# Kernel optimization log

Hardware: AMD Instinct MI355X
Metric: run time of the kernel (lower is better)

Reference implementation:

```python
import jax, jax.numpy as jnp
import numpy as np

B, N, C_IN, H, S, K = 32, 1024, 2, 32, 2, 2  # batch, nodes, input feat, hidden, n_supports, k_hop
NUM_MAT = S * K + 1  # identity + K hops per support


def setup_inputs() -> dict:
    key = jax.random.key(0)
    ks = jax.random.split(key, 6)
    inputs = jax.random.normal(ks[0], (B, N, C_IN), dtype=jnp.float32)
    # dense diffusion supports, scaled ~1/N so k-hop products stay O(1) (row-stochastic-like)
    supports = jax.random.uniform(ks[1], (B, S, N, N), dtype=jnp.float32) * (2.0 / N)
    states = jax.random.normal(ks[2], (B, N, H), dtype=jnp.float32)
    c_cat = C_IN + H
    scale = 1.0 / np.sqrt(NUM_MAT * c_cat)
    W_ru = jax.random.normal(ks[3], (NUM_MAT * c_cat, 2 * H), dtype=jnp.float32) * scale
    b_ru = jnp.zeros((2 * H,), dtype=jnp.float32)
    W_c = jax.random.normal(ks[4], (NUM_MAT * c_cat, H), dtype=jnp.float32) * scale
    b_c = jnp.zeros((H,), dtype=jnp.float32)
    return {"inputs": inputs, "supports": supports, "states": states,
            "W_ru": W_ru, "b_ru": b_ru, "W_c": W_c, "b_c": b_c}


def _graph_conv(x, supports, W, b):
    # x: [B,N,C]; supports: [B,S,N,N]. DCRNN dense diffusion conv:
    feats = [x]
    for s in range(S):
        A = supports[:, s]  # [B,N,N]
        xk = x
        for _ in range(K):
            xk = jnp.einsum('bnm,bmc->bnc', A, xk)
            feats.append(xk)
    h = jnp.concatenate(feats, axis=-1)  # [B,N,NUM_MAT*C]
    return jnp.einsum('bnf,fo->bno', h, W) + b


def reference(inputs, supports, states, W_ru, b_ru, W_c, b_c):
    r_u = jax.nn.sigmoid(_graph_conv(jnp.concatenate([inputs, states], -1), supports, W_ru, b_ru))
    r, u = r_u[..., :H], r_u[..., H:]
    c = jnp.tanh(_graph_conv(jnp.concatenate([inputs, r * states], -1), supports, W_c, b_c))
    outputs = u * states + (1.0 - u) * c
    return (outputs, outputs)
```

## Files before the change

### kernel.cpp

```cpp
#include <hip/hip_runtime.h>


#define NN   1024
#define HB   245760
#define SUBT 16384
#define OUTCOPY 1048576

typedef float  f32x4  __attribute__((ext_vector_type(4)));
typedef short  s16x4  __attribute__((ext_vector_type(4)));
typedef short  s16x8  __attribute__((ext_vector_type(8)));
typedef __bf16 bf16x8 __attribute__((ext_vector_type(8)));
typedef unsigned int u32x4 __attribute__((ext_vector_type(4)));

#define GAS __attribute__((address_space(1)))
#define LAS __attribute__((address_space(3)))

__device__ __forceinline__ unsigned short f32_bf16(float f) {
  unsigned int u = __float_as_uint(f);
  u += 0x7FFFu + ((u >> 16) & 1u);
  return (unsigned short)(u >> 16);
}
__device__ __forceinline__ float bf16_f32(unsigned short h) {
  return __uint_as_float(((unsigned int)h) << 16);
}

__device__ __forceinline__ void gload_lds16(const unsigned short* g, void* l) {
  __builtin_amdgcn_global_load_lds((const GAS void*)g, (LAS void*)l, 16, 0, 0);
}

__global__ __launch_bounds__(256)
void cvt_bf16(const float* __restrict__ src, unsigned short* __restrict__ dst, int n4) {
  int i = blockIdx.x * 256 + threadIdx.x;
  int stride = gridDim.x * 256;
  for (; i < n4; i += stride) {
    float4 v = ((const float4*)src)[i];
    s16x4 o;
    o.x = (short)f32_bf16(v.x);
    o.y = (short)f32_bf16(v.y);
    o.z = (short)f32_bf16(v.z);
    o.w = (short)f32_bf16(v.w);
    ((s16x4*)dst)[i] = o;
  }
}

__global__ __launch_bounds__(256)
void pack_x1(const float* __restrict__ inputs, const float* __restrict__ states,
             unsigned short* __restrict__ H1) {
  int gid = blockIdx.x * 256 + threadIdx.x;
  int b = gid >> 10, n = gid & 1023;
  unsigned short* xb = H1 + (size_t)b * HB;
  xb[0 * NN + n] = f32_bf16(inputs[gid * 2 + 0]);
  xb[1 * NN + n] = f32_bf16(inputs[gid * 2 + 1]);
#pragma unroll
  for (int o = 0; o < 32; ++o) {
    int ch = 2 + o;
    xb[(ch >> 4) * SUBT + (ch & 15) * NN + n] = f32_bf16(states[gid * 32 + o]);
  }
#pragma unroll
  for (int ch = 34; ch < 48; ++ch)
    xb[2 * SUBT + (ch & 15) * NN + n] = 0;
}

__global__ __launch_bounds__(256, 4)
void hop_fast(const unsigned short* __restrict__ Abf,
              const unsigned short* __restrict__ Hin,
              unsigned short* __restrict__ Hout,
              int si0, int si1, int so0, int so1) {
  __shared__ u32x4 lds4[2][896];

  const int tid  = threadIdx.x;
  const int wave = tid >> 6, lane = tid & 63;
  const int l15  = lane & 15,  l4  = lane >> 4;
  const int mblk = blockIdx.x, b = blockIdx.y, s = blockIdx.z;
  const int slot_in  = s ? si1 : si0;
  const int slot_out = s ? so1 : so0;

  const unsigned short* Xb = Hin  + (size_t)b * HB + (size_t)slot_in  * 3 * SUBT;
  unsigned short*       Yb = Hout + (size_t)b * HB + (size_t)slot_out * 3 * SUBT;
  const size_t arow0 = ((size_t)(b * 2 + s) * NN + (size_t)mblk * 64) * NN;

  f32x4 acc[3];
#pragma unroll
  for (int nt = 0; nt < 3; ++nt)
#pragma unroll
    for (int e = 0; e < 4; ++e) acc[nt][e] = 0.f;

  auto STAGE = [&](int bufi, int kb0) {
    char* base = (char*)&lds4[bufi][0];
#pragma unroll
    for (int i = 0; i < 2; ++i) {
      int q = i * 256 + tid;
      int r = q >> 3, cs = q & 7;
      const unsigned short* g = Abf + arow0 + (size_t)r * NN + kb0 + ((cs ^ (r & 7)) << 3);
      gload_lds16(g, base + (i * 256 + wave * 64) * 16);
    }
    {
      int q = tid;
      int ct = q >> 7, rem = q & 127, ch = rem >> 3, cs = rem & 7;
      const unsigned short* g = Xb + ct * SUBT + ch * NN + kb0 + ((cs ^ (ch & 7)) << 3);
      gload_lds16(g, base + 8192 + (wave * 64) * 16);
      if (wave < 2) {
        q = 256 + tid;
        ct = q >> 7; rem = q & 127; ch = rem >> 3; cs = rem & 7;
        g = Xb + ct * SUBT + ch * NN + kb0 + ((cs ^ (ch & 7)) << 3);
        gload_lds16(g, base + 8192 + (256 + wave * 64) * 16);
      }
    }
  };

  STAGE(0, 0);
  __syncthreads();

  const int row = wave * 16 + l15;
  const int sw  = (row & 7) << 4;
  const int swx = (l15 & 7) << 4;

  int cur = 0;
  for (int kt = 0; kt < 16; ++kt) {
    if (kt < 15) STAGE(cur ^ 1, (kt + 1) << 6);

    const char* lAb = (const char*)&lds4[cur][0];
    const char* lXb = lAb + 8192;

    __builtin_amdgcn_s_setprio(1);
#pragma unroll
    for (int kb = 0; kb < 2; ++kb) {
      const int ko = kb * 64 + (l4 << 3);
      s16x8 ta;
      ta.lo = *(const s16x4*)(lAb + row * 128 + (ko ^ sw));
      ta.hi = *(const s16x4*)(lAb + row * 128 + ((ko + 32) ^ sw));
      bf16x8 afr = __builtin_bit_cast(bf16x8, ta);
#pragma unroll
      for (int nt = 0; nt < 3; ++nt) {
        const char* bp = lXb + nt * 2048 + l15 * 128;
        s16x8 tb;
        tb.lo = *(const s16x4*)(bp + (ko ^ swx));
        tb.hi = *(const s16x4*)(bp + ((ko + 32) ^ swx));
        bf16x8 bfr = __builtin_bit_cast(bf16x8, tb);
        acc[nt] = __builtin_amdgcn_mfma_f32_16x16x32_bf16(afr, bfr, acc[nt], 0, 0, 0);
      }
    }
    __builtin_amdgcn_s_setprio(0);

    if (kt < 15) __syncthreads();
    cur ^= 1;
  }

  const int row0 = mblk * 64 + wave * 16 + (l4 << 2);
#pragma unroll
  for (int nt = 0; nt < 3; ++nt) {
    int ch = nt * 16 + l15;
    s16x4 o;
    o.x = (short)f32_bf16(acc[nt][0]);
    o.y = (short)f32_bf16(acc[nt][1]);
    o.z = (short)f32_bf16(acc[nt][2]);
    o.w = (short)f32_bf16(acc[nt][3]);
    *(s16x4*)(Yb + (size_t)ch * NN + row0) = o;
  }
}

__global__ __launch_bounds__(256)
void hop_slow(const float* __restrict__ Af32,
              const unsigned short* __restrict__ Hin,
              unsigned short* __restrict__ Hout,
              int si0, int si1, int so0, int so1) {
  __shared__ u32x4 lA4[1024];
  __shared__ u32x4 lX4[384];

  const int tid  = threadIdx.x;
  const int wave = tid >> 6, lane = tid & 63;
  const int l15  = lane & 15,  l4  = lane >> 4;
  const int mblk = blockIdx.x, b = blockIdx.y, s = blockIdx.z;
  const int slot_in  = s ? si1 : si0;
  const int slot_out = s ? so1 : so0;

  const unsigned short* Xb = Hin  + (size_t)b * HB + (size_t)slot_in  * 3 * SUBT;
  unsigned short*       Yb = Hout + (size_t)b * HB + (size_t)slot_out * 3 * SUBT;
  const size_t arow0 = ((size_t)(b * 2 + s) * NN + (size_t)mblk * 128) * NN;

  f32x4 acc[2][3];
#pragma unroll
  for (int mt = 0; mt < 2; ++mt)
#pragma unroll
    for (int nt = 0; nt < 3; ++nt)
#pragma unroll
      for (int e = 0; e < 4; ++e) acc[mt][nt][e] = 0.f;

  char* lAb = (char*)lA4;
  char* lXb = (char*)lX4;

  for (int kt = 0; kt < 16; ++kt) {
    const int kb0 = kt * 64;
    __syncthreads();
#pragma unroll
    for (int i = 0; i < 8; ++i) {
      int q = i * 256 + tid;
      int r = q >> 4, c = q & 15;
      float4 v = *(const float4*)(Af32 + arow0 + (size_t)r * NN + kb0 + c * 4);
      s16x4 o;
      o.x = (short)f32_bf16(v.x);
      o.y = (short)f32_bf16(v.y);
      o.z = (short)f32_bf16(v.z);
      o.w = (short)f32_bf16(v.w);
      *(s16x4*)(lAb + r * 128 + ((c * 8) ^ ((r & 7) << 4))) = o;
    }
    {
      int q = tid;
      int ct = q >> 7, rem = q & 127, ch = rem >> 3, c = rem & 7;
      const u32x4* src = (const u32x4*)(Xb + ct * SUBT + ch * NN + kb0 + c * 8);
      *(u32x4*)(lXb + ct * 2048 + ch * 128 + ((c ^ (ch & 7)) << 4)) = *src;
      if (tid < 128) {
        q = 256 + tid;
        ct = q >> 7; rem = q & 127; ch = rem >> 3; c = rem & 7;
        src = (const u32x4*)(Xb + ct * SUBT + ch * NN + kb0 + c * 8);
        *(u32x4*)(lXb + ct * 2048 + ch * 128 + ((c ^ (ch & 7)) << 4)) = *src;
      }
    }
    __syncthreads();
#pragma unroll
    for (int kb = 0; kb < 2; ++kb) {
      const int ko = kb * 64 + (l4 << 3);
      bf16x8 afr[2];
#pragma unroll
      for (int mt = 0; mt < 2; ++mt) {
        int row = wave * 32 + mt * 16 + l15;
        int sw  = (row & 7) << 4;
        s16x8 t;
        t.lo = *(const s16x4*)(lAb + row * 128 + (ko ^ sw));
        t.hi = *(const s16x4*)(lAb + row * 128 + ((ko + 32) ^ sw));
        afr[mt] = __builtin_bit_cast(bf16x8, t);
      }
#pragma unroll
      for (int nt = 0; nt < 3; ++nt) {
        const int swx = (l15 & 7) << 4;
        const char* bp = lXb + nt * 2048 + l15 * 128;
        s16x8 t;
        t.lo = *(const s16x4*)(bp + (ko ^ swx));
        t.hi = *(const s16x4*)(bp + ((ko + 32) ^ swx));
        bf16x8 bfr = __builtin_bit_cast(bf16x8, t);
#pragma unroll
        for (int mt = 0; mt < 2; ++mt)
          acc[mt][nt] = __builtin_amdgcn_mfma_f32_16x16x32_bf16(afr[mt], bfr, acc[mt][nt], 0, 0, 0);
      }
    }
  }

#pragma unroll
  for (int mt = 0; mt < 2; ++mt)
#pragma unroll
    for (int nt = 0; nt < 3; ++nt) {
      int ch   = nt * 16 + l15;
      int row0 = mblk * 128 + wave * 32 + mt * 16 + (l4 << 2);
      s16x4 o;
      o.x = (short)f32_bf16(acc[mt][nt][0]);
      o.y = (short)f32_bf16(acc[mt][nt][1]);
      o.z = (short)f32_bf16(acc[mt][nt][2]);
      o.w = (short)f32_bf16(acc[mt][nt][3]);
      *(s16x4*)(Yb + (size_t)ch * NN + row0) = o;
    }
}

__global__ __launch_bounds__(256)
void gate_ru(const unsigned short* __restrict__ H1,
             const float* __restrict__ W, const float* __restrict__ bias,
             const float* __restrict__ inputs, const float* __restrict__ states,
             unsigned short* __restrict__ H2, float* __restrict__ ubuf) {
  int gid = blockIdx.x * 256 + threadIdx.x;
  int b = gid >> 10, n = gid & 1023;
  const unsigned short* hb = H1 + (size_t)b * HB;
  float acc[64];
#pragma unroll
  for (int o = 0; o < 64; ++o) acc[o] = bias[o];
  for (int j = 0; j < 5; ++j) {
    const unsigned short* sb = hb + j * 3 * SUBT;
    for (int c = 0; c < 34; ++c) {
      float xv = bf16_f32(sb[(c >> 4) * SUBT + (c & 15) * NN + n]);
      const float* wr = W + (j * 34 + c) * 64;
#pragma unroll
      for (int o = 0; o < 64; ++o) acc[o] = fmaf(xv, wr[o], acc[o]);
    }
  }
  unsigned short* xb = H2 + (size_t)b * HB;
  xb[0 * NN + n] = f32_bf16(inputs[gid * 2 + 0]);
  xb[1 * NN + n] = f32_bf16(inputs[gid * 2 + 1]);
#pragma unroll
  for (int o = 0; o < 32; ++o) {
    float r = 1.f / (1.f + __expf(-acc[o]));
    float u = 1.f / (1.f + __expf(-acc[32 + o]));
    float sv = states[gid * 32 + o];
    int ch = 2 + o;
    xb[(ch >> 4) * SUBT + (ch & 15) * NN + n] = f32_bf16(r * sv);
    ubuf[((size_t)b * 32 + o) * NN + n] = u;
  }
#pragma unroll
  for (int ch = 34; ch < 48; ++ch)
    xb[2 * SUBT + (ch & 15) * NN + n] = 0;
}

__global__ __launch_bounds__(256)
void gate_c(const unsigned short* __restrict__ H2,
            const float* __restrict__ W, const float* __restrict__ bias,
            const float* __restrict__ states, const float* __restrict__ ubuf,
            float* __restrict__ out) {
  int gid = blockIdx.x * 256 + threadIdx.x;
  int b = gid >> 10, n = gid & 1023;
  const unsigned short* hb = H2 + (size_t)b * HB;
  float acc[32];
#pragma unroll
  for (int o = 0; o < 32; ++o) acc[o] = bias[o];
  for (int j = 0; j < 5; ++j) {
    const unsigned short* sb = hb + j * 3 * SUBT;
    for (int c = 0; c < 34; ++c) {
      float xv = bf16_f32(sb[(c >> 4) * SUBT + (c & 15) * NN + n]);
      const float* wr = W + (j * 34 + c) * 32;
#pragma unroll
      for (int o = 0; o < 32; ++o) acc[o] = fmaf(xv, wr[o], acc[o]);
    }
  }
  float res[32];
#pragma unroll
  for (int o = 0; o < 32; ++o) {
    float cc = tanhf(acc[o]);
    float u  = ubuf[((size_t)b * 32 + o) * NN + n];
    float sv = states[gid * 32 + o];
    res[o] = u * sv + (1.f - u) * cc;
  }
  float* o0 = out + (size_t)gid * 32;
#pragma unroll
  for (int q = 0; q < 8; ++q) {
    f32x4 v = { res[q * 4 + 0], res[q * 4 + 1], res[q * 4 + 2], res[q * 4 + 3] };
    *(f32x4*)(o0 + q * 4) = v;
    *(f32x4*)(o0 + OUTCOPY + q * 4) = v;
  }
}

extern "C" void kernel_launch(void* const* d_in, const int* in_sizes, int n_in,
                              void* d_out, int out_size, void* d_ws, size_t ws_size,
                              hipStream_t stream) {
  (void)in_sizes; (void)n_in; (void)out_size;
  const float* inputs   = (const float*)d_in[0];
  const float* supports = (const float*)d_in[1];
  const float* states   = (const float*)d_in[2];
  const float* W_ru     = (const float*)d_in[3];
  const float* b_ru     = (const float*)d_in[4];
  const float* W_c      = (const float*)d_in[5];
  const float* b_c      = (const float*)d_in[6];
  float* out = (float*)d_out;

  char* ws = (char*)d_ws;
  const size_t szA = 134217728;
  const size_t szH = 15728640;
  const size_t szU = 4194304;
  const bool pathA = ws_size >= szA + 2 * szH + szU;
  const size_t off = pathA ? szA : 0;

  unsigned short* Abf = (unsigned short*)ws;
  unsigned short* H1  = (unsigned short*)(ws + off);
  unsigned short* H2  = (unsigned short*)(ws + off + szH);
  float*          ub  = (float*)(ws + off + 2 * szH);

  dim3 fgrid(16, 32, 2), sgrid(8, 32, 2), blk(256);

  if (pathA)
    cvt_bf16<<<dim3(2048), blk, 0, stream>>>(supports, Abf, 16777216);

  pack_x1<<<dim3(128), blk, 0, stream>>>(inputs, states, H1);

  if (pathA) {
    hop_fast<<<fgrid, blk, 0, stream>>>(Abf, H1, H1, 0, 0, 1, 3);
    hop_fast<<<fgrid, blk, 0, stream>>>(Abf, H1, H1, 1, 3, 2, 4);
  } else {
    hop_slow<<<sgrid, blk, 0, stream>>>(supports, H1, H1, 0, 0, 1, 3);
    hop_slow<<<sgrid, blk, 0, stream>>>(supports, H1, H1, 1, 3, 2, 4);
  }

  gate_ru<<<dim3(128), blk, 0, stream>>>(H1, W_ru, b_ru, inputs, states, H2, ub);

  if (pathA) {
    hop_fast<<<fgrid, blk, 0, stream>>>(Abf, H2, H2, 0, 0, 1, 3);
    hop_fast<<<fgrid, blk, 0, stream>>>(Abf, H2, H2, 1, 3, 2, 4);
  } else {
    hop_slow<<<sgrid, blk, 0, stream>>>(supports, H2, H2, 0, 0, 1, 3);
    hop_slow<<<sgrid, blk, 0, stream>>>(supports, H2, H2, 1, 3, 2, 4);
  }

  gate_c<<<dim3(128), blk, 0, stream>>>(H2, W_c, b_c, states, ub, out);
}
```

Measured before the change: 320.6 us.

## Fuse all DCGRU stages into one persistent kernel with grid barriers

Replaces the sequence of separate launches (convert, pack, four hop GEMMs, two gate kernels) with a single persistent kernel of 256 blocks of 512 threads. The stages are separated by atomic-counter grid barriers. The hop phase now uses a 4-deep global-to-LDS pipeline with explicit waitcnt barriers, and each block computes two 128-row tiles. The gate stages are re-partitioned so that 8 threads share a node. The aim is to remove launch gaps and tail effects between the small kernels. The risks are deadlock if not all blocks are co-resident, spin-barrier overhead, and reduced occupancy.

```diff
diff --git a/kernel.cpp b/kernel.cpp
--- a/kernel.cpp
+++ b/kernel.cpp
@@ -23,23 +23,290 @@
 __device__ __forceinline__ float bf16_f32(unsigned short h) {
   return __uint_as_float(((unsigned int)h) << 16);
 }
-
 __device__ __forceinline__ void gload_lds16(const unsigned short* g, void* l) {
   __builtin_amdgcn_global_load_lds((const GAS void*)g, (LAS void*)l, 16, 0, 0);
 }
 
-__global__ __launch_bounds__(256)
-void cvt_bf16(const float* __restrict__ src, unsigned short* __restrict__ dst, int n4) {
-  int i = blockIdx.x * 256 + threadIdx.x;
-  int stride = gridDim.x * 256;
-  for (; i < n4; i += stride) {
-    float4 v = ((const float4*)src)[i];
-    s16x4 o;
-    o.x = (short)f32_bf16(v.x);
-    o.y = (short)f32_bf16(v.y);
-    o.z = (short)f32_bf16(v.z);
-    o.w = (short)f32_bf16(v.w);
-    ((s16x4*)dst)[i] = o;
+#define WB(N) do {                                              \
+    asm volatile("s_waitcnt vmcnt(" #N ") lgkmcnt(0)" ::: "memory"); \
+    __builtin_amdgcn_s_barrier();                               \
+    __builtin_amdgcn_sched_barrier(0);                          \
+  } while (0)
+
+__device__ __forceinline__ void gbar(unsigned* bar, unsigned target) {
+  __syncthreads();
+  if (threadIdx.x == 0) {
+    __threadfence();
+    __hip_atomic_fetch_add(bar, 1u, __ATOMIC_RELAXED, __HIP_MEMORY_SCOPE_AGENT);
+    unsigned v;
+    do {
+      __builtin_amdgcn_s_sleep(8);
+      v = __hip_atomic_load(bar, __ATOMIC_RELAXED, __HIP_MEMORY_SCOPE_AGENT);
+    } while (v < target);
+    __threadfence();
+  }
+  __syncthreads();
+}
+
+__device__ void hop_phase(const unsigned short* __restrict__ Abf,
+                          const unsigned short* __restrict__ Hin,
+                          unsigned short* __restrict__ Hout,
+                          int bs, int m0, char* lds,
+                          int si0, int si1, int so0, int so1) {
+  const int tid  = threadIdx.x;
+  const int wave = tid >> 6, lane = tid & 63;
+  const int l15  = lane & 15, l4 = lane >> 4;
+  const int b = bs & 31, s = bs >> 5;
+  const int slot_in  = s ? si1 : si0;
+  const int slot_out = s ? so1 : so0;
+
+  const unsigned short* Xb = Hin  + (size_t)b * HB + (size_t)slot_in  * 3 * SUBT;
+  unsigned short*       Yb = Hout + (size_t)b * HB + (size_t)slot_out * 3 * SUBT;
+  const size_t a0 = ((size_t)(b * 2 + s) * NN + (size_t)m0 * 128) * NN;
+  const size_t a1 = a0 + (size_t)4 * 128 * NN;
+
+  auto ISSUE = [&](int t) {
+    const int kt = t & 15, kb0 = kt << 6;
+    const size_t ar = (t >> 4) ? a1 : a0;
+    char* base = lds + (t & 3) * 24576;
+#pragma unroll
+    for (int i = 0; i < 2; ++i) {
+      int q = i * 512 + tid;
+      int r = q >> 3, cs = q & 7;
+      gload_lds16(Abf + ar + (size_t)r * NN + kb0 + ((cs ^ (r & 7)) << 3),
+                  base + (i * 512 + wave * 64) * 16);
+    }
+    {
+      int q = tid;
+      int ct = q >> 7, ch = (q >> 3) & 15, cs = q & 7;
+      gload_lds16(Xb + ct * SUBT + ch * NN + kb0 + ((cs ^ (ch & 7)) << 3),
+                  base + 16384 + (wave * 64) * 16);
+    }
+  };
+
+  const int row = wave * 16 + l15;
+  const int sw  = (row & 7) << 4;
+  const int swx = (l15 & 7) << 4;
+
+  f32x4 acc[3];
+#pragma unroll
+  for (int nt = 0; nt < 3; ++nt)
+#pragma unroll
+    for (int e = 0; e < 4; ++e) acc[nt][e] = 0.f;
+  s16x4 sv0[3];
+
+  auto COMPUTE = [&](int t) {
+    const char* lAb = lds + (t & 3) * 24576;
+    const char* lXb = lAb + 16384;
+#pragma unroll
+    for (int kb = 0; kb < 2; ++kb) {
+      const int ko = kb * 64 + (l4 << 3);
+      s16x8 ta;
+      ta.lo = *(const s16x4*)(lAb + row * 128 + (ko ^ sw));
+      ta.hi = *(const s16x4*)(lAb + row * 128 + ((ko + 32) ^ sw));
+      bf16x8 afr = __builtin_bit_cast(bf16x8, ta);
+#pragma unroll
+      for (int nt = 0; nt < 3; ++nt) {
+        const char* bp = lXb + nt * 2048 + l15 * 128;
+        s16x8 tb;
+        tb.lo = *(const s16x4*)(bp + (ko ^ swx));
+        tb.hi = *(const s16x4*)(bp + ((ko + 32) ^ swx));
+        bf16x8 bfr = __builtin_bit_cast(bf16x8, tb);
+        acc[nt] = __builtin_amdgcn_mfma_f32_16x16x32_bf16(afr, bfr, acc[nt], 0, 0, 0);
+      }
+    }
+  };
+
+  auto PACK = [&](s16x4* dst) {
+#pragma unroll
+    for (int nt = 0; nt < 3; ++nt) {
+      dst[nt].x = (short)f32_bf16(acc[nt][0]);
+      dst[nt].y = (short)f32_bf16(acc[nt][1]);
+      dst[nt].z = (short)f32_bf16(acc[nt][2]);
+      dst[nt].w = (short)f32_bf16(acc[nt][3]);
+    }
+  };
+
+  ISSUE(0); ISSUE(1); ISSUE(2);
+
+#pragma unroll 1
+  for (int k = 0; k < 30; ++k) {
+    WB(6);
+    if (k < 29) ISSUE(k + 3);
+    COMPUTE(k);
+    if (k == 15) {
+      PACK(sv0);
+#pragma unroll
+      for (int nt = 0; nt < 3; ++nt)
+#pragma unroll
+        for (int e = 0; e < 4; ++e) acc[nt][e] = 0.f;
+    }
+  }
+  WB(3); COMPUTE(30);
+  WB(0); COMPUTE(31);
+
+  s16x4 sv1[3];
+  PACK(sv1);
+
+  const int r0 = m0 * 128 + wave * 16 + (l4 << 2);
+  const int r1 = (m0 + 4) * 128 + wave * 16 + (l4 << 2);
+#pragma unroll
+  for (int nt = 0; nt < 3; ++nt) {
+    int ch = nt * 16 + l15;
+    *(s16x4*)(Yb + (size_t)ch * NN + r0) = sv0[nt];
+    *(s16x4*)(Yb + (size_t)ch * NN + r1) = sv1[nt];
+  }
+}
+
+__global__ __launch_bounds__(512, 2)
+void dcgru_fused(const float* __restrict__ inputs, const float* __restrict__ supports,
+                 const float* __restrict__ states,
+                 const float* __restrict__ W_ru, const float* __restrict__ b_ru,
+                 const float* __restrict__ W_c,  const float* __restrict__ b_c,
+                 float* __restrict__ out,
+                 unsigned short* __restrict__ Abf,
+                 unsigned short* __restrict__ H1, unsigned short* __restrict__ H2,
+                 float* __restrict__ ubuf, unsigned* bar) {
+  __shared__ u32x4 ldsv[6144];
+  char* lds = (char*)ldsv;
+
+  const int tid = threadIdx.x;
+  const int gid = blockIdx.x * 512 + tid;
+
+  const int x  = blockIdx.x & 7;
+  const int j  = blockIdx.x >> 3;
+  const int bs = x * 8 + (j >> 2);
+  const int m0 = j & 3;
+
+  {
+    const f32x4* src = (const f32x4*)supports;
+#pragma unroll 1
+    for (int i = gid; i < 16777216; i += 524288) {
+      f32x4 v0 = __builtin_nontemporal_load(src + i);
+      f32x4 v1 = __builtin_nontemporal_load(src + i + 131072);
+      f32x4 v2 = __builtin_nontemporal_load(src + i + 262144);
+      f32x4 v3 = __builtin_nontemporal_load(src + i + 393216);
+      s16x4 o0 = { (short)f32_bf16(v0[0]), (short)f32_bf16(v0[1]), (short)f32_bf16(v0[2]), (short)f32_bf16(v0[3]) };
+      s16x4 o1 = { (short)f32_bf16(v1[0]), (short)f32_bf16(v1[1]), (short)f32_bf16(v1[2]), (short)f32_bf16(v1[3]) };
+      s16x4 o2 = { (short)f32_bf16(v2[0]), (short)f32_bf16(v2[1]), (short)f32_bf16(v2[2]), (short)f32_bf16(v2[3]) };
+      s16x4 o3 = { (short)f32_bf16(v3[0]), (short)f32_bf16(v3[1]), (short)f32_bf16(v3[2]), (short)f32_bf16(v3[3]) };
+      ((s16x4*)Abf)[i] = o0;
+      ((s16x4*)Abf)[i + 131072] = o1;
+      ((s16x4*)Abf)[i + 262144] = o2;
+      ((s16x4*)Abf)[i + 393216] = o3;
+    }
+    if (gid < 32768) {
+      int b = gid >> 10, n = gid & 1023;
+      unsigned short* xb = H1 + (size_t)b * HB;
+      xb[0 * NN + n] = f32_bf16(inputs[gid * 2 + 0]);
+      xb[1 * NN + n] = f32_bf16(inputs[gid * 2 + 1]);
+#pragma unroll
+      for (int o = 0; o < 32; ++o) {
+        int ch = 2 + o;
+        xb[(ch >> 4) * SUBT + (ch & 15) * NN + n] = f32_bf16(states[gid * 32 + o]);
+      }
+#pragma unroll
+      for (int ch = 34; ch < 48; ++ch)
+        xb[2 * SUBT + (ch & 15) * NN + n] = 0;
+    }
+  }
+  gbar(bar, 256);
+
+  hop_phase(Abf, H1, H1, bs, m0, lds, 0, 0, 1, 3);
+  gbar(bar, 512);
+  hop_phase(Abf, H1, H1, bs, m0, lds, 1, 3, 2, 4);
+  gbar(bar, 768);
+
+  {
+#pragma unroll 1
+    for (int rep = 0; rep < 2; ++rep) {
+      int tau = gid + rep * 131072;
+      int rw = tau >> 3, p = tau & 7;
+      int b = rw >> 10, n = rw & 1023;
+      const unsigned short* hb = H1 + (size_t)b * HB;
+      float acc[8];
+#pragma unroll
+      for (int q = 0; q < 8; ++q) acc[q] = b_ru[p * 8 + q];
+#pragma unroll 1
+      for (int jj = 0; jj < 5; ++jj) {
+        const unsigned short* sb = hb + jj * 3 * SUBT;
+#pragma unroll 1
+        for (int c = 0; c < 34; ++c) {
+          float xv = bf16_f32(sb[(c >> 4) * SUBT + (c & 15) * NN + n]);
+          const float* wr = W_ru + (jj * 34 + c) * 64 + p * 8;
+          f32x4 w0 = *(const f32x4*)wr;
+          f32x4 w1 = *(const f32x4*)(wr + 4);
+#pragma unroll
+          for (int q = 0; q < 4; ++q) acc[q]     = fmaf(xv, w0[q], acc[q]);
+#pragma unroll
+          for (int q = 0; q < 4; ++q) acc[4 + q] = fmaf(xv, w1[q], acc[4 + q]);
+        }
+      }
+      unsigned short* xb = H2 + (size_t)b * HB;
+      if (p < 4) {
+#pragma unroll
+        for (int q = 0; q < 8; ++q) {
+          float r = 1.f / (1.f + __expf(-acc[q]));
+          int o = p * 8 + q, ch = 2 + o;
+          xb[(ch >> 4) * SUBT + (ch & 15) * NN + n] = f32_bf16(r * states[rw * 32 + o]);
+        }
+      } else {
+        int mm = (p - 4) * 8;
+#pragma unroll
+        for (int q = 0; q < 8; ++q) {
+          float u = 1.f / (1.f + __expf(-acc[q]));
+          ubuf[((size_t)b * 32 + mm + q) * NN + n] = u;
+        }
+      }
+      if (p == 4) { for (int ch = 34; ch < 41; ++ch) xb[2 * SUBT + (ch & 15) * NN + n] = 0; }
+      if (p == 5) { for (int ch = 41; ch < 48; ++ch) xb[2 * SUBT + (ch & 15) * NN + n] = 0; }
+      if (p == 6) {
+        xb[0 * NN + n] = f32_bf16(inputs[rw * 2 + 0]);
+        xb[1 * NN + n] = f32_bf16(inputs[rw * 2 + 1]);
+      }
+    }
+  }
+  gbar(bar, 1024);
+
+  hop_phase(Abf, H2, H2, bs, m0, lds, 0, 0, 1, 3);
+  gbar(bar, 1280);
+  hop_phase(Abf, H2, H2, bs, m0, lds, 1, 3, 2, 4);
+  gbar(bar, 1536);
+
+  {
+#pragma unroll 1
+    for (int rep = 0; rep < 2; ++rep) {
+      int tau = gid + rep * 131072;
+      int rw = tau >> 3, p = tau & 7;
+      int b = rw >> 10, n = rw & 1023;
+      const unsigned short* hb = H2 + (size_t)b * HB;
+      float acc[4];
+#pragma unroll
+      for (int q = 0; q < 4; ++q) acc[q] = b_c[p * 4 + q];
+#pragma unroll 1
+      for (int jj = 0; jj < 5; ++jj) {
+        const unsigned short* sb = hb + jj * 3 * SUBT;
+#pragma unroll 1
+        for (int c = 0; c < 34; ++c) {
+          float xv = bf16_f32(sb[(c >> 4) * SUBT + (c & 15) * NN + n]);
+          f32x4 w0 = *(const f32x4*)(W_c + (jj * 34 + c) * 32 + p * 4);
+#pragma unroll
+          for (int q = 0; q < 4; ++q) acc[q] = fmaf(xv, w0[q], acc[q]);
+        }
+      }
+      f32x4 res;
+#pragma unroll
+      for (int q = 0; q < 4; ++q) {
+        int o = p * 4 + q;
+        float cc = tanhf(acc[q]);
+        float u  = ubuf[((size_t)b * 32 + o) * NN + n];
+        float sv = states[rw * 32 + o];
+        res[q] = u * sv + (1.f - u) * cc;
+      }
+      float* o0 = out + (size_t)rw * 32 + p * 4;
+      *(f32x4*)o0 = res;
+      *(f32x4*)(o0 + OUTCOPY) = res;
+    }
   }
 }
 
@@ -61,104 +328,6 @@
     xb[2 * SUBT + (ch & 15) * NN + n] = 0;
 }
 
-__global__ __launch_bounds__(256, 4)
-void hop_fast(const unsigned short* __restrict__ Abf,
-              const unsigned short* __restrict__ Hin,
-              unsigned short* __restrict__ Hout,
-              int si0, int si1, int so0, int so1) {
-  __shared__ u32x4 lds4[2][896];
-
-  const int tid  = threadIdx.x;
-  const int wave = tid >> 6, lane = tid & 63;
-  const int l15  = lane & 15,  l4  = lane >> 4;
-  const int mblk = blockIdx.x, b = blockIdx.y, s = blockIdx.z;
-  const int slot_in  = s ? si1 : si0;
-  const int slot_out = s ? so1 : so0;
-
-  const unsigned short* Xb = Hin  + (size_t)b * HB + (size_t)slot_in  * 3 * SUBT;
-  unsigned short*       Yb = Hout + (size_t)b * HB + (size_t)slot_out * 3 * SUBT;
-  const size_t arow0 = ((size_t)(b * 2 + s) * NN + (size_t)mblk * 64) * NN;
-
-  f32x4 acc[3];
-#pragma unroll
-  for (int nt = 0; nt < 3; ++nt)
-#pragma unroll
-    for (int e = 0; e < 4; ++e) acc[nt][e] = 0.f;
-
-  auto STAGE = [&](int bufi, int kb0) {
-    char* base = (char*)&lds4[bufi][0];
-#pragma unroll
-    for (int i = 0; i < 2; ++i) {
-      int q = i * 256 + tid;
-      int r = q >> 3, cs = q & 7;
-      const unsigned short* g = Abf + arow0 + (size_t)r * NN + kb0 + ((cs ^ (r & 7)) << 3);
-      gload_lds16(g, base + (i * 256 + wave * 64) * 16);
-    }
-    {
-      int q = tid;
-      int ct = q >> 7, rem = q & 127, ch = rem >> 3, cs = rem & 7;
-      const unsigned short* g = Xb + ct * SUBT + ch * NN + kb0 + ((cs ^ (ch & 7)) << 3);
-      gload_lds16(g, base + 8192 + (wave * 64) * 16);
-      if (wave < 2) {
-        q = 256 + tid;
-        ct = q >> 7; rem = q & 127; ch = rem >> 3; cs = rem & 7;
-        g = Xb + ct * SUBT + ch * NN + kb0 + ((cs ^ (ch & 7)) << 3);
-        gload_lds16(g, base + 8192 + (256 + wave * 64) * 16);
-      }
-    }
-  };
-
-  STAGE(0, 0);
-  __syncthreads();
-
-  const int row = wave * 16 + l15;
-  const int sw  = (row & 7) << 4;
-  const int swx = (l15 & 7) << 4;
-
-  int cur = 0;
-  for (int kt = 0; kt < 16; ++kt) {
-    if (kt < 15) STAGE(cur ^ 1, (kt + 1) << 6);
-
-    const char* lAb = (const char*)&lds4[cur][0];
-    const char* lXb = lAb + 8192;
-
-    __builtin_amdgcn_s_setprio(1);
-#pragma unroll
-    for (int kb = 0; kb < 2; ++kb) {
-      const int ko = kb * 64 + (l4 << 3);
-      s16x8 ta;
-      ta.lo = *(const s16x4*)(lAb + row * 128 + (ko ^ sw));
-      ta.hi = *(const s16x4*)(lAb + row * 128 + ((ko + 32) ^ sw));
-      bf16x8 afr = __builtin_bit_cast(bf16x8, ta);
-#pragma unroll
-      for (int nt = 0; nt < 3; ++nt) {
-        const char* bp = lXb + nt * 2048 + l15 * 128;
-        s16x8 tb;
-        tb.lo = *(const s16x4*)(bp + (ko ^ swx));
-        tb.hi = *(const s16x4*)(bp + ((ko + 32) ^ swx));
-        bf16x8 bfr = __builtin_bit_cast(bf16x8, tb);
-        acc[nt] = __builtin_amdgcn_mfma_f32_16x16x32_bf16(afr, bfr, acc[nt], 0, 0, 0);
-      }
-    }
-    __builtin_amdgcn_s_setprio(0);
-
-    if (kt < 15) __syncthreads();
-    cur ^= 1;
-  }
-
-  const int row0 = mblk * 64 + wave * 16 + (l4 << 2);
-#pragma unroll
-  for (int nt = 0; nt < 3; ++nt) {
-    int ch = nt * 16 + l15;
-    s16x4 o;
-    o.x = (short)f32_bf16(acc[nt][0]);
-    o.y = (short)f32_bf16(acc[nt][1]);
-    o.z = (short)f32_bf16(acc[nt][2]);
-    o.w = (short)f32_bf16(acc[nt][3]);
-    *(s16x4*)(Yb + (size_t)ch * NN + row0) = o;
-  }
-}
-
 __global__ __launch_bounds__(256)
 void hop_slow(const float* __restrict__ Af32,
               const unsigned short* __restrict__ Hin,
@@ -166,18 +335,15 @@
               int si0, int si1, int so0, int so1) {
   __shared__ u32x4 lA4[1024];
   __shared__ u32x4 lX4[384];
-
   const int tid  = threadIdx.x;
   const int wave = tid >> 6, lane = tid & 63;
   const int l15  = lane & 15,  l4  = lane >> 4;
   const int mblk = blockIdx.x, b = blockIdx.y, s = blockIdx.z;
   const int slot_in  = s ? si1 : si0;
   const int slot_out = s ? so1 : so0;
-
   const unsigned short* Xb = Hin  + (size_t)b * HB + (size_t)slot_in  * 3 * SUBT;
   unsigned short*       Yb = Hout + (size_t)b * HB + (size_t)slot_out * 3 * SUBT;
   const size_t arow0 = ((size_t)(b * 2 + s) * NN + (size_t)mblk * 128) * NN;
-
   f32x4 acc[2][3];
 #pragma unroll
   for (int mt = 0; mt < 2; ++mt)
@@ -185,10 +351,8 @@
     for (int nt = 0; nt < 3; ++nt)
 #pragma unroll
       for (int e = 0; e < 4; ++e) acc[mt][nt][e] = 0.f;
-
   char* lAb = (char*)lA4;
   char* lXb = (char*)lX4;
-
   for (int kt = 0; kt < 16; ++kt) {
     const int kb0 = kt * 64;
     __syncthreads();
@@ -198,10 +362,8 @@
       int r = q >> 4, c = q & 15;
       float4 v = *(const float4*)(Af32 + arow0 + (size_t)r * NN + kb0 + c * 4);
       s16x4 o;
-      o.x = (short)f32_bf16(v.x);
-      o.y = (short)f32_bf16(v.y);
-      o.z = (short)f32_bf16(v.z);
-      o.w = (short)f32_bf16(v.w);
+      o.x = (short)f32_bf16(v.x); o.y = (short)f32_bf16(v.y);
+      o.z = (short)f32_bf16(v.z); o.w = (short)f32_bf16(v.w);
       *(s16x4*)(lAb + r * 128 + ((c * 8) ^ ((r & 7) << 4))) = o;
     }
     {
@@ -244,7 +406,6 @@
       }
     }
   }
-
 #pragma unroll
   for (int mt = 0; mt < 2; ++mt)
 #pragma unroll
@@ -252,19 +413,17 @@
       int ch   = nt * 16 + l15;
       int row0 = mblk * 128 + wave * 32 + mt * 16 + (l4 << 2);
       s16x4 o;
-      o.x = (short)f32_bf16(acc[mt][nt][0]);
-      o.y = (short)f32_bf16(acc[mt][nt][1]);
-      o.z = (short)f32_bf16(acc[mt][nt][2]);
-      o.w = (short)f32_bf16(acc[mt][nt][3]);
+      o.x = (short)f32_bf16(acc[mt][nt][0]); o.y = (short)f32_bf16(acc[mt][nt][1]);
+      o.z = (short)f32_bf16(acc[mt][nt][2]); o.w = (short)f32_bf16(acc[mt][nt][3]);
       *(s16x4*)(Yb + (size_t)ch * NN + row0) = o;
     }
 }
 
 __global__ __launch_bounds__(256)
-void gate_ru(const unsigned short* __restrict__ H1,
-             const float* __restrict__ W, const float* __restrict__ bias,
-             const float* __restrict__ inputs, const float* __restrict__ states,
-             unsigned short* __restrict__ H2, float* __restrict__ ubuf) {
+void gate_ru_k(const unsigned short* __restrict__ H1,
+               const float* __restrict__ W, const float* __restrict__ bias,
+               const float* __restrict__ inputs, const float* __restrict__ states,
+               unsigned short* __restrict__ H2, float* __restrict__ ubuf) {
   int gid = blockIdx.x * 256 + threadIdx.x;
   int b = gid >> 10, n = gid & 1023;
   const unsigned short* hb = H1 + (size_t)b * HB;
@@ -287,9 +446,8 @@
   for (int o = 0; o < 32; ++o) {
     float r = 1.f / (1.f + __expf(-acc[o]));
     float u = 1.f / (1.f + __expf(-acc[32 + o]));
-    float sv = states[gid * 32 + o];
     int ch = 2 + o;
-    xb[(ch >> 4) * SUBT + (ch & 15) * NN + n] = f32_bf16(r * sv);
+    xb[(ch >> 4) * SUBT + (ch & 15) * NN + n] = f32_bf16(r * states[gid * 32 + o]);
     ubuf[((size_t)b * 32 + o) * NN + n] = u;
   }
 #pragma unroll
@@ -298,10 +456,10 @@
 }
 
 __global__ __launch_bounds__(256)
-void gate_c(const unsigned short* __restrict__ H2,
-            const float* __restrict__ W, const float* __restrict__ bias,
-            const float* __restrict__ states, const float* __restrict__ ubuf,
-            float* __restrict__ out) {
+void gate_c_k(const unsigned short* __restrict__ H2,
+              const float* __restrict__ W, const float* __restrict__ bias,
+              const float* __restrict__ states, const float* __restrict__ ubuf,
+              float* __restrict__ out) {
   int gid = blockIdx.x * 256 + threadIdx.x;
   int b = gid >> 10, n = gid & 1023;
   const unsigned short* hb = H2 + (size_t)b * HB;
@@ -351,38 +509,29 @@
   const size_t szA = 134217728;
   const size_t szH = 15728640;
   const size_t szU = 4194304;
-  const bool pathA = ws_size >= szA + 2 * szH + szU;
-  const size_t off = pathA ? szA : 0;
-
-  unsigned short* Abf = (unsigned short*)ws;
-  unsigned short* H1  = (unsigned short*)(ws + off);
-  unsigned short* H2  = (unsigned short*)(ws + off + szH);
-  float*          ub  = (float*)(ws + off + 2 * szH);
-
-  dim3 fgrid(16, 32, 2), sgrid(8, 32, 2), blk(256);
-
-  if (pathA)
-    cvt_bf16<<<dim3(2048), blk, 0, stream>>>(supports, Abf, 16777216);
-
-  pack_x1<<<dim3(128), blk, 0, stream>>>(inputs, states, H1);
-
-  if (pathA) {
-    hop_fast<<<fgrid, blk, 0, stream>>>(Abf, H1, H1, 0, 0, 1, 3);
-    hop_fast<<<fgrid, blk, 0, stream>>>(Abf, H1, H1, 1, 3, 2, 4);
+  const size_t BAR_OFF = szA + 2 * szH + szU;
+  const bool pathF = ws_size >= BAR_OFF + 256;
+
+  if (pathF) {
+    unsigned short* Abf = (unsigned short*)ws;
+    unsigned short* H1  = (unsigned short*)(ws + szA);
+    unsigned short* H2  = (unsigned short*)(ws + szA + szH);
+    float*          ub  = (float*)(ws + szA + 2 * szH);
+    unsigned*       bar = (unsigned*)(ws + BAR_OFF);
+    hipMemsetAsync(bar, 0, 256, stream);
+    dcgru_fused<<<dim3(256), dim3(512), 0, stream>>>(
+        inputs, supports, states, W_ru, b_ru, W_c, b_c, out, Abf, H1, H2, ub, bar);
   } else {
+    unsigned short* H1 = (unsigned short*)ws;
+    unsigned short* H2 = (unsigned short*)(ws + szH);
+    float*          ub = (float*)(ws + 2 * szH);
+    dim3 sgrid(8, 32, 2), blk(256);
+    pack_x1<<<dim3(128), blk, 0, stream>>>(inputs, states, H1);
     hop_slow<<<sgrid, blk, 0, stream>>>(supports, H1, H1, 0, 0, 1, 3);
     hop_slow<<<sgrid, blk, 0, stream>>>(supports, H1, H1, 1, 3, 2, 4);
-  }
-
-  gate_ru<<<dim3(128), blk, 0, stream>>>(H1, W_ru, b_ru, inputs, states, H2, ub);
-
-  if (pathA) {
-    hop_fast<<<fgrid, blk, 0, stream>>>(Abf, H2, H2, 0, 0, 1, 3);
-    hop_fast<<<fgrid, blk, 0, stream>>>(Abf, H2, H2, 1, 3, 2, 4);
-  } else {
+    gate_ru_k<<<dim3(128), blk, 0, stream>>>(H1, W_ru, b_ru, inputs, states, H2, ub);
     hop_slow<<<sgrid, blk, 0, stream>>>(supports, H2, H2, 0, 0, 1, 3);
     hop_slow<<<sgrid, blk, 0, stream>>>(supports, H2, H2, 1, 3, 2, 4);
-  }
-
-  gate_c<<<dim3(128), blk, 0, stream>>>(H2, W_c, b_c, states, ub, out);
-}
+    gate_c_k<<<dim3(128), blk, 0, stream>>>(H2, W_c, b_c, states, ub, out);
+  }
+}
```

After: 468.8 us. 46.2% more time.
